# Kernel optimization log

Measured on AMD Instinct MI355X. Metric: run time of the kernel, lower is better.

## Reference

```python
import jax, jax.numpy as jnp
import numpy as np

E, P, K, V, H, NE = 768, 256, 32, 32, 128, 8
B, M_DIM, T_DIM = 16, 4, 512


def setup_inputs() -> dict:
    key = jax.random.key(0)
    ks = jax.random.split(key, 24)
    s = 0.05
    inp = {
        'token_embeddings': jax.random.normal(ks[0], (B, M_DIM, T_DIM, E), jnp.float32),
        'U': jax.random.uniform(ks[1], (B, M_DIM, T_DIM), jnp.float32),
        'R': jax.random.uniform(ks[2], (B, M_DIM, M_DIM, T_DIM), jnp.float32),
        'S': jax.random.uniform(ks[3], (B, M_DIM, M_DIM, T_DIM), jnp.float32),
        'W_tp': jax.random.normal(ks[4], (E, P), jnp.float32) * s,
        'b_tp': jnp.zeros((P,), jnp.float32),
        'W_q': jax.random.normal(ks[5], (P, K), jnp.float32) * s,
        'b_q': jnp.zeros((K,), jnp.float32),
        'W_k': jax.random.normal(ks[6], (2, K), jnp.float32) * s,
        'b_k': jnp.zeros((K,), jnp.float32),
        'W_v': jax.random.normal(ks[7], (2, V), jnp.float32) * s,
        'b_v': jnp.zeros((V,), jnp.float32),
        'W_ih': jax.random.normal(ks[8], (3 * H, 1 + V), jnp.float32) * s,
        'W_hh': jax.random.normal(ks[9], (3 * H, H), jnp.float32) * s,
        'b_ih': jnp.zeros((3 * H,), jnp.float32),
        'b_hh': jnp.zeros((3 * H,), jnp.float32),
        'W1': jax.random.normal(ks[10], (P + H, (P + H) // 2), jnp.float32) * s,
        'b1': jnp.zeros(((P + H) // 2,), jnp.float32),
        'W2': jax.random.normal(ks[11], ((P + H) // 2, NE), jnp.float32) * s,
        'b2': jnp.zeros((NE,), jnp.float32),
        'M': M_DIM,
        'T': T_DIM,
    }
    return inp


def _gru(x, W_ih, W_hh, b_ih, b_hh):
    # x: [N, T, D] -> outputs [N, T, H]; PyTorch GRU cell math
    N, T, _ = x.shape
    Hh = W_hh.shape[1]
    gi = jnp.einsum('ntd,gd->ntg', x, W_ih) + b_ih  # [N,T,3H] precomputed input gates
    gi = jnp.transpose(gi, (1, 0, 2))  # [T,N,3H]

    def step(h, gi_t):
        gh = h @ W_hh.T + b_hh
        i_r, i_z, i_n = jnp.split(gi_t, 3, axis=-1)
        h_r, h_z, h_n = jnp.split(gh, 3, axis=-1)
        r = jax.nn.sigmoid(i_r + h_r)
        z = jax.nn.sigmoid(i_z + h_z)
        n = jnp.tanh(i_n + r * h_n)
        h_new = (1.0 - z) * n + z * h
        return h_new, h_new

    h0 = jnp.zeros((N, Hh), x.dtype)
    _, hs = jax.lax.scan(step, h0, gi)
    return jnp.transpose(hs, (1, 0, 2))  # [N,T,H]


def reference(token_embeddings, U, R, S, W_tp, b_tp, W_q, b_q, W_k, b_k, W_v, b_v,
              W_ih, W_hh, b_ih, b_hh, W1, b1, W2, b2, M, T):
    Bn, Mn, Tn, _ = token_embeddings.shape
    proc = jax.nn.relu(token_embeddings @ W_tp + b_tp)           # [B,M,T,P]
    query = proc @ W_q + b_q                                     # [B,M,T,K]
    Rp = jnp.transpose(R, (0, 3, 1, 2))                          # [B,T,M,M]
    Sp = jnp.transpose(S, (0, 3, 1, 2))
    pf = jnp.stack([Rp, Sp], axis=-1)                            # [B,T,M,M,2]
    keys = pf @ W_k + b_k                                        # [B,T,M,M,K]
    vals = pf @ W_v + b_v                                        # [B,T,M,M,V]
    scores = jnp.einsum('bmtk,btmjk->bmtj', query, keys) / np.sqrt(K)
    diag = jnp.eye(Mn, dtype=bool)                               # exclude j == m
    scores = jnp.where(diag[None, :, None, :], -1e9, scores)
    w = jax.nn.softmax(scores, axis=-1)                          # [B,M,T,M]
    ctx = jnp.einsum('bmtj,btmjv->bmtv', w, vals)                # [B,M,T,V]
    gru_in = jnp.concatenate([U[..., None], ctx], axis=-1)       # [B,M,T,1+V]
    gru_out = _gru(gru_in.reshape(Bn * Mn, Tn, 1 + V), W_ih, W_hh, b_ih, b_hh)
    rus_ctx = gru_out.reshape(Bn, Mn, Tn, H)
    combined = jnp.concatenate([proc, rus_ctx], axis=-1)         # [B,M,T,P+H]
    hidden = jax.nn.relu(combined @ W1 + b1)
    logits = hidden @ W2 + b2                                    # [B,M,T,NE]
    return logits
```

## Files before the change

kernel.cpp:

```cpp
#include <hip/hip_runtime.h>


typedef __attribute__((ext_vector_type(8))) short short8;
typedef __attribute__((ext_vector_type(4))) float f32x4;

__device__ __forceinline__ float bf2f(unsigned short u) {
    return __uint_as_float(((unsigned int)u) << 16);
}
__device__ __forceinline__ unsigned short f2bf(float f) {
    unsigned int x = __float_as_uint(f);
    return (unsigned short)((x + 0x7FFFu + ((x >> 16) & 1u)) >> 16);
}
__device__ __forceinline__ float sigm(float x) { return 1.0f / (1.0f + __expf(-x)); }
__device__ __forceinline__ float tanh_fast(float x) {
    x = fminf(fmaxf(x, -15.0f), 15.0f);
    float e = __expf(-2.0f * x);
    return (1.0f - e) / (1.0f + e);
}
__device__ __forceinline__ float dpp_xor1_add(float v) {
    int o = __builtin_amdgcn_update_dpp(0, __float_as_int(v), 0xB1, 0xF, 0xF, true);
    return v + __int_as_float(o);
}
__device__ __forceinline__ float sel4(f32x4 c, int sel) {
    float t0 = (sel & 1) ? c[1] : c[0];
    float t1 = (sel & 1) ? c[3] : c[2];
    return (sel & 2) ? t1 : t0;
}

#define CST_SC   768
#define CST_WU   800
#define CST_WA2  1184
#define CST_WB2  1568
#define CST_CC   1952

__global__ void k_paint(float* out, float val, int nmax) {
    int i = blockIdx.x * blockDim.x + threadIdx.x;
    if (i < nmax) out[i] = val;
}

__global__ void k_prep(const float* __restrict__ Wq,
                       const float* __restrict__ bq,
                       const float* __restrict__ Wk,
                       const float* __restrict__ bk,
                       const float* __restrict__ Wv,
                       const float* __restrict__ bv,
                       const float* __restrict__ Wih,
                       const float* __restrict__ bih,
                       float* __restrict__ cst)
{
    const int t = threadIdx.x;
    if (t < 256) {
        float a = 0.f, b = 0.f, c = 0.f;
        for (int k = 0; k < 32; ++k) {
            float w = Wq[t * 32 + k];
            a = fmaf(w, Wk[k], a);
            b = fmaf(w, Wk[32 + k], b);
            c = fmaf(w, bk[k], c);
        }
        cst[t] = a; cst[256 + t] = b; cst[512 + t] = c;
    }
    if (t == 0) {
        float ca = 0.f, cb = 0.f, cc = 0.f;
        for (int k = 0; k < 32; ++k) {
            float bqk = bq[k];
            ca = fmaf(bqk, Wk[k], ca);
            cb = fmaf(bqk, Wk[32 + k], cb);
            cc = fmaf(bqk, bk[k], cc);
        }
        cst[CST_SC + 0] = ca; cst[CST_SC + 1] = cb; cst[CST_SC + 2] = cc;
    }
    if (t < 384) {
        cst[CST_WU + t] = Wih[t * 33];
        float a2 = 0.f, b2 = 0.f, c2 = bih[t];
        for (int v = 0; v < 32; ++v) {
            float w = Wih[t * 33 + 1 + v];
            a2 = fmaf(w, Wv[v], a2);
            b2 = fmaf(w, Wv[32 + v], b2);
            c2 = fmaf(w, bv[v], c2);
        }
        cst[CST_WA2 + t] = a2; cst[CST_WB2 + t] = b2; cst[CST_CC + t] = c2;
    }
}

__global__ __launch_bounds__(256) void k_proc(
    const float* __restrict__ A,
    const float* __restrict__ Bw,
    const float* __restrict__ bias,
    unsigned short* __restrict__ C)
{
    __shared__ unsigned short A_s[64 * 40];
    __shared__ unsigned short B_s[64 * 40];
    const int t = threadIdx.x;
    const int row0 = blockIdx.y * 64;
    const int col0 = blockIdx.x * 64;
    const int lane = t & 63, wave = t >> 6;
    const int wr = wave >> 1, wc = wave & 1;
    const int quad = lane >> 4, l16 = lane & 15;

    f32x4 acc[2][2] = {};

    for (int k0 = 0; k0 < 768; k0 += 32) {
        {
            const int r = t >> 2, kq = (t & 3) * 8;
            const float* src = A + (size_t)(row0 + r) * 768 + k0 + kq;
            float4 v0 = *(const float4*)(src);
            float4 v1 = *(const float4*)(src + 4);
            short8 s;
            s[0] = f2bf(v0.x); s[1] = f2bf(v0.y); s[2] = f2bf(v0.z); s[3] = f2bf(v0.w);
            s[4] = f2bf(v1.x); s[5] = f2bf(v1.y); s[6] = f2bf(v1.z); s[7] = f2bf(v1.w);
            *(short8*)(A_s + r * 40 + kq) = s;
        }
        {
            const int k = t >> 3, nq = (t & 7) * 8;
            const float* src = Bw + (size_t)(k0 + k) * 256 + col0 + nq;
            float4 v0 = *(const float4*)(src);
            float4 v1 = *(const float4*)(src + 4);
            B_s[(nq + 0) * 40 + k] = f2bf(v0.x);
            B_s[(nq + 1) * 40 + k] = f2bf(v0.y);
            B_s[(nq + 2) * 40 + k] = f2bf(v0.z);
            B_s[(nq + 3) * 40 + k] = f2bf(v0.w);
            B_s[(nq + 4) * 40 + k] = f2bf(v1.x);
            B_s[(nq + 5) * 40 + k] = f2bf(v1.y);
            B_s[(nq + 6) * 40 + k] = f2bf(v1.z);
            B_s[(nq + 7) * 40 + k] = f2bf(v1.w);
        }
        __syncthreads();
        short8 af[2], bf[2];
        #pragma unroll
        for (int im = 0; im < 2; ++im)
            af[im] = *(const short8*)(A_s + (wr * 32 + im * 16 + l16) * 40 + quad * 8);
        #pragma unroll
        for (int in = 0; in < 2; ++in)
            bf[in] = *(const short8*)(B_s + (wc * 32 + in * 16 + l16) * 40 + quad * 8);
        #pragma unroll
        for (int im = 0; im < 2; ++im)
            #pragma unroll
            for (int in = 0; in < 2; ++in)
                acc[im][in] = __builtin_amdgcn_mfma_f32_16x16x32_bf16(
                    af[im], bf[in], acc[im][in], 0, 0, 0);
        __syncthreads();
    }
    float bias_v[2];
    #pragma unroll
    for (int in = 0; in < 2; ++in) bias_v[in] = bias[col0 + wc * 32 + in * 16 + l16];
    #pragma unroll
    for (int im = 0; im < 2; ++im)
        #pragma unroll
        for (int in = 0; in < 2; ++in) {
            const int c_g = col0 + wc * 32 + in * 16 + l16;
            #pragma unroll
            for (int reg = 0; reg < 4; ++reg) {
                const int r_g = row0 + wr * 32 + im * 16 + quad * 4 + reg;
                float v = fmaxf(acc[im][in][reg] + bias_v[in], 0.f);
                C[(size_t)r_g * 256 + c_g] = f2bf(v);
            }
        }
}

__global__ __launch_bounds__(256) void k_attn(
    const unsigned short* __restrict__ proc,
    const float* __restrict__ R,
    const float* __restrict__ S,
    const float* __restrict__ cst,
    float* __restrict__ wrws)
{
    __shared__ float wv_s[768];
    const int tid = threadIdx.x;
    for (int i = tid; i < 768; i += 256) wv_s[i] = cst[i];
    __syncthreads();

    const int lane = tid & 63, wave = tid >> 6;
    const int row = blockIdx.x * 4 + wave;
    const int t = row & 511, m = (row >> 9) & 3, b = row >> 11;
    const int p0 = lane * 4;

    ushort4 u = *(const ushort4*)(proc + (size_t)row * 256 + p0);
    float p0f = bf2f(u.x), p1f = bf2f(u.y), p2f = bf2f(u.z), p3f = bf2f(u.w);
    float dA = 0.f, dB = 0.f, dC = 0.f;
    dA = fmaf(p0f, wv_s[p0 + 0], dA); dB = fmaf(p0f, wv_s[256 + p0 + 0], dB); dC = fmaf(p0f, wv_s[512 + p0 + 0], dC);
    dA = fmaf(p1f, wv_s[p0 + 1], dA); dB = fmaf(p1f, wv_s[256 + p0 + 1], dB); dC = fmaf(p1f, wv_s[512 + p0 + 1], dC);
    dA = fmaf(p2f, wv_s[p0 + 2], dA); dB = fmaf(p2f, wv_s[256 + p0 + 2], dB); dC = fmaf(p2f, wv_s[512 + p0 + 2], dC);
    dA = fmaf(p3f, wv_s[p0 + 3], dA); dB = fmaf(p3f, wv_s[256 + p0 + 3], dB); dC = fmaf(p3f, wv_s[512 + p0 + 3], dC);
    #pragma unroll
    for (int mm = 1; mm < 64; mm <<= 1) {
        dA += __shfl_xor(dA, mm, 64);
        dB += __shfl_xor(dB, mm, 64);
        dC += __shfl_xor(dC, mm, 64);
    }
    if (lane == 0) {
        dA += cst[CST_SC + 0]; dB += cst[CST_SC + 1]; dC += cst[CST_SC + 2];
        const float scale = 0.17677669529663687f;
        float rr[4], ss[4], sc[4], mx = -1e30f;
        #pragma unroll
        for (int j = 0; j < 4; ++j) {
            const size_t idx = ((size_t)(b * 16 + m * 4 + j)) * 512 + t;
            rr[j] = R[idx]; ss[j] = S[idx];
            float v = (rr[j] * dA + ss[j] * dB + dC) * scale;
            if (j == m) v = -1e9f;
            sc[j] = v; mx = fmaxf(mx, v);
        }
        float w[4], se = 0.f;
        #pragma unroll
        for (int j = 0; j < 4; ++j) { w[j] = __expf(sc[j] - mx); se += w[j]; }
        const float inv = 1.0f / se;
        float wr = 0.f, wss = 0.f;
        #pragma unroll
        for (int j = 0; j < 4; ++j) { wr += w[j] * rr[j]; wss += w[j] * ss[j]; }
        float2 o; o.x = wr * inv; o.y = wss * inv;
        ((float2*)wrws)[row] = o;
    }
}

__global__ __launch_bounds__(512) void k_gru(
    const float* __restrict__ wrws,
    const float* __restrict__ U,
    const float* __restrict__ Whh,
    const float* __restrict__ bhh,
    const float* __restrict__ cst,
    unsigned short* __restrict__ gout)
{
    __shared__ unsigned short hbuf[2][2][144];
    __shared__ float4 uvw_s[512];

    const int tid  = threadIdx.x;
    const int lane = tid & 63, w = tid >> 6;
    const int l16  = lane & 15, quad = lane >> 4;
    const int n    = blockIdx.x;
    const int par  = l16 & 1;
    const int sel  = (l16 >> 1) & 3;
    const int eg   = 16 * w + quad * 4 + sel;
    const bool writer = (l16 < 8) && ((l16 & 1) == 0);

    short8 afr[3][4];
    #pragma unroll
    for (int g3 = 0; g3 < 3; ++g3) {
        const int row = g3 * 128 + 16 * w + l16;
        const float* rp = Whh + (size_t)row * 128 + quad * 8;
        #pragma unroll
        for (int kf = 0; kf < 4; ++kf) {
            float4 v0 = *(const float4*)(rp + kf * 32);
            float4 v1 = *(const float4*)(rp + kf * 32 + 4);
            short8 s;
            s[0] = f2bf(v0.x); s[1] = f2bf(v0.y); s[2] = f2bf(v0.z); s[3] = f2bf(v0.w);
            s[4] = f2bf(v1.x); s[5] = f2bf(v1.y); s[6] = f2bf(v1.z); s[7] = f2bf(v1.w);
            afr[g3][kf] = s;
        }
    }

    const float wu_r = cst[CST_WU  + eg], wu_z = cst[CST_WU  + 128 + eg], wu_n = cst[CST_WU  + 256 + eg];
    const float wa_r = cst[CST_WA2 + eg], wa_z = cst[CST_WA2 + 128 + eg], wa_n = cst[CST_WA2 + 256 + eg];
    const float wb_r = cst[CST_WB2 + eg], wb_z = cst[CST_WB2 + 128 + eg], wb_n = cst[CST_WB2 + 256 + eg];
    const float cc_r = cst[CST_CC  + eg] + bhh[eg];
    const float cc_z = cst[CST_CC  + 128 + eg] + bhh[128 + eg];
    const float cc_n = cst[CST_CC  + 256 + eg];
    const float bh_n = bhh[256 + eg];

    {
        float u = U[(size_t)n * 512 + tid];
        float2 w2 = ((const float2*)wrws)[(size_t)n * 512 + tid];
        float4 p; p.x = u; p.y = w2.x; p.z = w2.y; p.w = 0.f;
        uvw_s[tid] = p;
    }
    if (tid < 288) ((unsigned int*)hbuf)[tid] = 0u;
    __syncthreads();

    float h_old = 0.f;
    const f32x4 ZZ = {0.f, 0.f, 0.f, 0.f};

    for (int t = 0; t < 512; ++t) {
        const int cur = t & 1, nxt = cur ^ 1;

        const unsigned short* hb = &hbuf[cur][par][0];
        short8 bfr[4];
        #pragma unroll
        for (int kf = 0; kf < 4; ++kf)
            bfr[kf] = *(const short8*)(hb + kf * 32 + quad * 8);
        const float4 uvw = uvw_s[t];

        f32x4 c0 = ZZ, c1 = ZZ, c2 = ZZ;
        #pragma unroll
        for (int kf = 0; kf < 4; ++kf) {
            c0 = __builtin_amdgcn_mfma_f32_16x16x32_bf16(afr[0][kf], bfr[kf], c0, 0, 0, 0);
            c1 = __builtin_amdgcn_mfma_f32_16x16x32_bf16(afr[1][kf], bfr[kf], c1, 0, 0, 0);
            c2 = __builtin_amdgcn_mfma_f32_16x16x32_bf16(afr[2][kf], bfr[kf], c2, 0, 0, 0);
        }

        const float ghr = dpp_xor1_add(sel4(c0, sel));
        const float ghz = dpp_xor1_add(sel4(c1, sel));
        const float ghn = dpp_xor1_add(sel4(c2, sel)) + bh_n;

        const float gir = fmaf(uvw.z, wb_r, fmaf(uvw.y, wa_r, fmaf(uvw.x, wu_r, cc_r)));
        const float giz = fmaf(uvw.z, wb_z, fmaf(uvw.y, wa_z, fmaf(uvw.x, wu_z, cc_z)));
        const float gin = fmaf(uvw.z, wb_n, fmaf(uvw.y, wa_n, fmaf(uvw.x, wu_n, cc_n)));
        const float r  = sigm(gir + ghr);
        const float z  = sigm(giz + ghz);
        const float nn = tanh_fast(fmaf(r, ghn, gin));
        const float hn = fmaf(z, h_old - nn, nn);
        h_old = hn;

        if (writer) {
            const unsigned short hi16 = f2bf(hn);
            hbuf[nxt][0][eg] = hi16;
            hbuf[nxt][1][eg] = f2bf(hn - bf2f(hi16));
            gout[((size_t)n * 512 + t) * 128 + eg] = hi16;
        }
        asm volatile("s_waitcnt lgkmcnt(0)" ::: "memory");
        __builtin_amdgcn_s_barrier();
        asm volatile("" ::: "memory");
        __builtin_amdgcn_sched_barrier(0);
    }
}

__global__ __launch_bounds__(256) void k_hid(
    const unsigned short* __restrict__ proc,
    const unsigned short* __restrict__ gout,
    const float* __restrict__ W1,
    const float* __restrict__ b1,
    const float* __restrict__ W2,
    const float* __restrict__ b2,
    float* __restrict__ out)
{
    __shared__ float smem[14088];
    float* As  = smem;
    float* Bs  = smem + 1088;
    float* Hs  = smem;
    float* W2s = smem + 12544;
    float* b2s = smem + 14080;
    const int tid = threadIdx.x;
    const int row0 = blockIdx.x * 64;
    for (int i = tid; i < 1536; i += 256) W2s[i] = W2[i];
    if (tid < 8) b2s[tid] = b2[tid];
    const int ty = tid >> 4, tx = tid & 15;
    const int ar = tid >> 2, akq = (tid & 3) * 4;
    const int bkr = tid >> 4, bc0 = (tid & 15) * 12;
    float acc[4][12] = {};

    for (int k0 = 0; k0 < 384; k0 += 16) {
        {
            const int kk = k0 + akq;
            ushort4 u;
            if (kk < 256) u = *(const ushort4*)(proc + (size_t)(row0 + ar) * 256 + kk);
            else          u = *(const ushort4*)(gout + (size_t)(row0 + ar) * 128 + (kk - 256));
            As[ar * 17 + akq + 0] = bf2f(u.x); As[ar * 17 + akq + 1] = bf2f(u.y);
            As[ar * 17 + akq + 2] = bf2f(u.z); As[ar * 17 + akq + 3] = bf2f(u.w);
        }
        {
            const float* wsrc = W1 + (size_t)(k0 + bkr) * 192 + bc0;
            #pragma unroll
            for (int q = 0; q < 3; ++q) {
                float4 w4 = *(const float4*)(wsrc + 4 * q);
                Bs[bkr * 192 + bc0 + 4 * q + 0] = w4.x;
                Bs[bkr * 192 + bc0 + 4 * q + 1] = w4.y;
                Bs[bkr * 192 + bc0 + 4 * q + 2] = w4.z;
                Bs[bkr * 192 + bc0 + 4 * q + 3] = w4.w;
            }
        }
        __syncthreads();
        #pragma unroll
        for (int k = 0; k < 16; ++k) {
            float a[4], bb[12];
            #pragma unroll
            for (int i = 0; i < 4; ++i) a[i] = As[(ty * 4 + i) * 17 + k];
            #pragma unroll
            for (int j = 0; j < 12; ++j) bb[j] = Bs[k * 192 + tx * 12 + j];
            #pragma unroll
            for (int i = 0; i < 4; ++i)
                #pragma unroll
                for (int j = 0; j < 12; ++j)
                    acc[i][j] = fmaf(a[i], bb[j], acc[i][j]);
        }
        __syncthreads();
    }
    #pragma unroll
    for (int i = 0; i < 4; ++i)
        #pragma unroll
        for (int j = 0; j < 12; ++j) {
            const int c = tx * 12 + j;
            Hs[(ty * 4 + i) * 196 + c] = fmaxf(acc[i][j] + b1[c], 0.f);
        }
    __syncthreads();
    const int r = tid >> 2, qq = tid & 3;
    const int e0 = 2 * qq, e1 = 2 * qq + 1;
    float s0 = b2s[e0], s1 = b2s[e1];
    for (int c = 0; c < 192; ++c) {
        float h = Hs[r * 196 + c];
        s0 = fmaf(h, W2s[c * 8 + e0], s0);
        s1 = fmaf(h, W2s[c * 8 + e1], s1);
    }
    out[(size_t)(row0 + r) * 8 + e0] = s0;
    out[(size_t)(row0 + r) * 8 + e1] = s1;
}

extern "C" void kernel_launch(void* const* d_in, const int* in_sizes, int n_in,
                              void* d_out, int out_size, void* d_ws, size_t ws_size,
                              hipStream_t stream) {
    const float* emb  = (const float*)d_in[0];
    const float* U    = (const float*)d_in[1];
    const float* R    = (const float*)d_in[2];
    const float* S    = (const float*)d_in[3];
    const float* W_tp = (const float*)d_in[4];
    const float* b_tp = (const float*)d_in[5];
    const float* W_q  = (const float*)d_in[6];
    const float* b_q  = (const float*)d_in[7];
    const float* W_k  = (const float*)d_in[8];
    const float* b_k  = (const float*)d_in[9];
    const float* W_v  = (const float*)d_in[10];
    const float* b_v  = (const float*)d_in[11];
    const float* W_ih = (const float*)d_in[12];
    const float* W_hh = (const float*)d_in[13];
    const float* b_ih = (const float*)d_in[14];
    const float* b_hh = (const float*)d_in[15];
    const float* W1   = (const float*)d_in[16];
    const float* b1   = (const float*)d_in[17];
    const float* W2   = (const float*)d_in[18];
    const float* b2   = (const float*)d_in[19];

    float* outp = (float*)d_out;

    const size_t NEEDED = 25444352u;
    if (ws_size < NEEDED) {
        k_paint<<<(out_size + 255) / 256, 256, 0, stream>>>(outp, 3.0f, out_size);
        return;
    }

    char* ws = (char*)d_ws;
    unsigned short* proc = (unsigned short*)(ws);
    float*          wrws = (float*)(ws + 16777216u);
    unsigned short* gout = (unsigned short*)(ws + 17039360u);
    float*          cst  = (float*)(ws + 25427968u);

    k_prep<<<1, 512, 0, stream>>>(W_q, b_q, W_k, b_k, W_v, b_v, W_ih, b_ih, cst);
    k_proc<<<dim3(4, 512), 256, 0, stream>>>(emb, W_tp, b_tp, proc);
    k_attn<<<8192, 256, 0, stream>>>(proc, R, S, cst, wrws);
    k_gru <<<64, 512, 0, stream>>>(wrws, U, W_hh, b_hh, cst, gout);
    k_hid <<<512, 256, 0, stream>>>(proc, gout, W1, b1, W2, b2, outp);
}
```

Baseline: 608.1 us.

## Halve GRU block to 4 waves, each computing 32 hidden units with six MFMAs

The recurrent GRU kernel now runs with 256 threads (4 waves) instead of 512. Each wave holds two 16-row slices of W_hh per gate and issues six MFMAs per k-step, so all lanes with even parity now write a hidden unit. The aim is to cut per-step barrier cost and wave synchronisation on the serial time loop. In exchange it doubles per-wave MFMA work and register pressure for the weight fragments. It also unrolls the time loop by two and relaxes the scheduling barrier mask.

```diff
diff --git a/kernel.cpp b/kernel.cpp
--- a/kernel.cpp
+++ b/kernel.cpp
@@ -211,7 +211,7 @@
     }
 }
 
-__global__ __launch_bounds__(512) void k_gru(
+__global__ __launch_bounds__(256) void k_gru(
     const float* __restrict__ wrws,
     const float* __restrict__ U,
     const float* __restrict__ Whh,
@@ -228,24 +228,27 @@
     const int n    = blockIdx.x;
     const int par  = l16 & 1;
     const int sel  = (l16 >> 1) & 3;
-    const int eg   = 16 * w + quad * 4 + sel;
-    const bool writer = (l16 < 8) && ((l16 & 1) == 0);
-
-    short8 afr[3][4];
+    const int hh   = (l16 >> 3) & 1;
+    const int eg   = 32 * w + 16 * hh + quad * 4 + sel;
+    const bool writer = (par == 0);
+
+    short8 afr[3][2][4];
     #pragma unroll
-    for (int g3 = 0; g3 < 3; ++g3) {
-        const int row = g3 * 128 + 16 * w + l16;
-        const float* rp = Whh + (size_t)row * 128 + quad * 8;
-        #pragma unroll
-        for (int kf = 0; kf < 4; ++kf) {
-            float4 v0 = *(const float4*)(rp + kf * 32);
-            float4 v1 = *(const float4*)(rp + kf * 32 + 4);
-            short8 s;
-            s[0] = f2bf(v0.x); s[1] = f2bf(v0.y); s[2] = f2bf(v0.z); s[3] = f2bf(v0.w);
-            s[4] = f2bf(v1.x); s[5] = f2bf(v1.y); s[6] = f2bf(v1.z); s[7] = f2bf(v1.w);
-            afr[g3][kf] = s;
-        }
-    }
+    for (int g3 = 0; g3 < 3; ++g3)
+        #pragma unroll
+        for (int h2 = 0; h2 < 2; ++h2) {
+            const int row = g3 * 128 + 32 * w + 16 * h2 + l16;
+            const float* rp = Whh + (size_t)row * 128 + quad * 8;
+            #pragma unroll
+            for (int kf = 0; kf < 4; ++kf) {
+                float4 v0 = *(const float4*)(rp + kf * 32);
+                float4 v1 = *(const float4*)(rp + kf * 32 + 4);
+                short8 s;
+                s[0] = f2bf(v0.x); s[1] = f2bf(v0.y); s[2] = f2bf(v0.z); s[3] = f2bf(v0.w);
+                s[4] = f2bf(v1.x); s[5] = f2bf(v1.y); s[6] = f2bf(v1.z); s[7] = f2bf(v1.w);
+                afr[g3][h2][kf] = s;
+            }
+        }
 
     const float wu_r = cst[CST_WU  + eg], wu_z = cst[CST_WU  + 128 + eg], wu_n = cst[CST_WU  + 256 + eg];
     const float wa_r = cst[CST_WA2 + eg], wa_z = cst[CST_WA2 + 128 + eg], wa_n = cst[CST_WA2 + 256 + eg];
@@ -255,18 +258,19 @@
     const float cc_n = cst[CST_CC  + 256 + eg];
     const float bh_n = bhh[256 + eg];
 
-    {
-        float u = U[(size_t)n * 512 + tid];
-        float2 w2 = ((const float2*)wrws)[(size_t)n * 512 + tid];
+    for (int i = tid; i < 512; i += 256) {
+        float u = U[(size_t)n * 512 + i];
+        float2 w2 = ((const float2*)wrws)[(size_t)n * 512 + i];
         float4 p; p.x = u; p.y = w2.x; p.z = w2.y; p.w = 0.f;
-        uvw_s[tid] = p;
-    }
-    if (tid < 288) ((unsigned int*)hbuf)[tid] = 0u;
+        uvw_s[i] = p;
+    }
+    for (int i = tid; i < 288; i += 256) ((unsigned int*)hbuf)[i] = 0u;
     __syncthreads();
 
     float h_old = 0.f;
     const f32x4 ZZ = {0.f, 0.f, 0.f, 0.f};
 
+    #pragma unroll 2
     for (int t = 0; t < 512; ++t) {
         const int cur = t & 1, nxt = cur ^ 1;
 
@@ -277,24 +281,28 @@
             bfr[kf] = *(const short8*)(hb + kf * 32 + quad * 8);
         const float4 uvw = uvw_s[t];
 
-        f32x4 c0 = ZZ, c1 = ZZ, c2 = ZZ;
-        #pragma unroll
-        for (int kf = 0; kf < 4; ++kf) {
-            c0 = __builtin_amdgcn_mfma_f32_16x16x32_bf16(afr[0][kf], bfr[kf], c0, 0, 0, 0);
-            c1 = __builtin_amdgcn_mfma_f32_16x16x32_bf16(afr[1][kf], bfr[kf], c1, 0, 0, 0);
-            c2 = __builtin_amdgcn_mfma_f32_16x16x32_bf16(afr[2][kf], bfr[kf], c2, 0, 0, 0);
-        }
-
-        const float ghr = dpp_xor1_add(sel4(c0, sel));
-        const float ghz = dpp_xor1_add(sel4(c1, sel));
-        const float ghn = dpp_xor1_add(sel4(c2, sel)) + bh_n;
+        f32x4 c[6] = {ZZ, ZZ, ZZ, ZZ, ZZ, ZZ};
+        #pragma unroll
+        for (int kf = 0; kf < 4; ++kf)
+            #pragma unroll
+            for (int j = 0; j < 6; ++j)
+                c[j] = __builtin_amdgcn_mfma_f32_16x16x32_bf16(
+                    afr[j >> 1][j & 1][kf], bfr[kf], c[j], 0, 0, 0);
+
+        float gh[3];
+        #pragma unroll
+        for (int g3 = 0; g3 < 3; ++g3) {
+            const float v0 = sel4(c[2 * g3 + 0], sel);
+            const float v1 = sel4(c[2 * g3 + 1], sel);
+            gh[g3] = dpp_xor1_add(hh ? v1 : v0);
+        }
 
         const float gir = fmaf(uvw.z, wb_r, fmaf(uvw.y, wa_r, fmaf(uvw.x, wu_r, cc_r)));
         const float giz = fmaf(uvw.z, wb_z, fmaf(uvw.y, wa_z, fmaf(uvw.x, wu_z, cc_z)));
         const float gin = fmaf(uvw.z, wb_n, fmaf(uvw.y, wa_n, fmaf(uvw.x, wu_n, cc_n)));
-        const float r  = sigm(gir + ghr);
-        const float z  = sigm(giz + ghz);
-        const float nn = tanh_fast(fmaf(r, ghn, gin));
+        const float r  = sigm(gir + gh[0]);
+        const float z  = sigm(giz + gh[1]);
+        const float nn = tanh_fast(fmaf(r, gh[2] + bh_n, gin));
         const float hn = fmaf(z, h_old - nn, nn);
         h_old = hn;
 
@@ -307,7 +315,7 @@
         asm volatile("s_waitcnt lgkmcnt(0)" ::: "memory");
         __builtin_amdgcn_s_barrier();
         asm volatile("" ::: "memory");
-        __builtin_amdgcn_sched_barrier(0);
+        __builtin_amdgcn_sched_barrier(0x7);
     }
 }
 
@@ -432,6 +440,6 @@
     k_prep<<<1, 512, 0, stream>>>(W_q, b_q, W_k, b_k, W_v, b_v, W_ih, b_ih, cst);
     k_proc<<<dim3(4, 512), 256, 0, stream>>>(emb, W_tp, b_tp, proc);
     k_attn<<<8192, 256, 0, stream>>>(proc, R, S, cst, wrws);
-    k_gru <<<64, 512, 0, stream>>>(wrws, U, W_hh, b_hh, cst, gout);
+    k_gru <<<64, 256, 0, stream>>>(wrws, U, W_hh, b_hh, cst, gout);
     k_hid <<<512, 256, 0, stream>>>(proc, gout, W1, b1, W2, b2, outp);
 }
```

After: 584.3 us. 3.9% less time.
